# Kernel tuning notes

Measured on AMD Instinct MI355X. Metric: run time of the kernel, lower is better.

## Reference

```python
import jax, jax.numpy as jnp
import numpy as np

B, P, ENC = 64, 196, 2048
ATT, DEC, EMB = 512, 512, 512
V, MAXLEN = 10000, 30


def setup_inputs() -> dict:
    key = jax.random.key(0)
    ks = jax.random.split(key, 20)
    s = 0.02
    inp = {
        "encoder_out": jax.random.normal(ks[0], (B, P, ENC), jnp.float32),
        "captions": jax.random.randint(ks[1], (B, MAXLEN), 0, V).astype(jnp.int64),
        "caption_lengths": jax.random.randint(ks[2], (B,), 1, MAXLEN).astype(jnp.int64),
        # parameters (PyTorch Linear convention: y = x @ W.T + b)
        "emb_table": jax.random.uniform(ks[3], (V, EMB), jnp.float32, -0.1, 0.1),
        "W_enc_att": jax.random.normal(ks[4], (ATT, ENC), jnp.float32) * s,
        "b_enc_att": jnp.zeros((ATT,), jnp.float32),
        "W_dec_att": jax.random.normal(ks[5], (ATT, DEC), jnp.float32) * s,
        "b_dec_att": jnp.zeros((ATT,), jnp.float32),
        "w_full_att": jax.random.normal(ks[6], (1, ATT), jnp.float32) * s,
        "b_full_att": jnp.zeros((1,), jnp.float32),
        "W_ih": jax.random.normal(ks[7], (4 * DEC, EMB + ENC), jnp.float32) * s,
        "b_ih": jnp.zeros((4 * DEC,), jnp.float32),
        "W_hh": jax.random.normal(ks[8], (4 * DEC, DEC), jnp.float32) * s,
        "b_hh": jnp.zeros((4 * DEC,), jnp.float32),
        "W_init_h": jax.random.normal(ks[9], (DEC, ENC), jnp.float32) * s,
        "b_init_h": jnp.zeros((DEC,), jnp.float32),
        "W_init_c": jax.random.normal(ks[10], (DEC, ENC), jnp.float32) * s,
        "b_init_c": jnp.zeros((DEC,), jnp.float32),
        "W_fc": jax.random.uniform(ks[11], (V, DEC), jnp.float32, -0.1, 0.1),
        "b_fc": jnp.zeros((V,), jnp.float32),
    }
    return inp


def reference(encoder_out, captions, caption_lengths, emb_table,
              W_enc_att, b_enc_att, W_dec_att, b_dec_att,
              w_full_att, b_full_att, W_ih, b_ih, W_hh, b_hh,
              W_init_h, b_init_h, W_init_c, b_init_c, W_fc, b_fc):
    # init hidden state from mean-pooled encoder features
    mean_enc = encoder_out.mean(axis=1)                       # [B, ENC]
    h0 = mean_enc @ W_init_h.T + b_init_h                     # [B, DEC]
    c0 = mean_enc @ W_init_c.T + b_init_c                     # [B, DEC]

    # encoder-side attention projection is time-invariant: hoist out of the loop
    att1 = jnp.einsum('bpe,ae->bpa', encoder_out, W_enc_att) + b_enc_att  # [B, P, ATT]

    embeddings = emb_table[captions]                          # [B, T, EMB]
    T = captions.shape[1] - 1
    emb_steps = jnp.swapaxes(embeddings[:, :T, :], 0, 1)      # [T, B, EMB]

    def step(carry, emb_t):
        h, c = carry
        att2 = h @ W_dec_att.T + b_dec_att                    # [B, ATT]
        e = (jax.nn.relu(att1 + att2[:, None, :]) @ w_full_att.T + b_full_att)[..., 0]  # [B, P]
        alpha = jax.nn.softmax(e, axis=1)                     # [B, P]
        context = jnp.einsum('bp,bpe->be', alpha, encoder_out)  # [B, ENC]
        x = jnp.concatenate([emb_t, context], axis=1)         # [B, EMB+ENC]
        gates = x @ W_ih.T + b_ih + h @ W_hh.T + b_hh         # [B, 4*DEC]
        i, f, g, o = jnp.split(gates, 4, axis=1)
        c_new = jax.nn.sigmoid(f) * c + jax.nn.sigmoid(i) * jnp.tanh(g)
        h_new = jax.nn.sigmoid(o) * jnp.tanh(c_new)
        preds = h_new @ W_fc.T + b_fc                         # dropout in eval mode = identity
        return (h_new, c_new), (preds, alpha)

    _, (preds_seq, alpha_seq) = jax.lax.scan(step, (h0, c0), emb_steps)
    predictions = jnp.swapaxes(preds_seq, 0, 1)               # [B, T, V]
    alphas = jnp.swapaxes(alpha_seq, 0, 1)                    # [B, T, P]
    return predictions, alphas
```

## Files before the change

kernel.cpp:

```cpp
#include <hip/hip_runtime.h>
#include <cstddef>

constexpr int B_   = 64;
constexpr int P_   = 196;
constexpr int ENC_ = 2048;
constexpr int ATT_ = 512;
constexpr int DEC_ = 512;
constexpr int EMB_ = 512;
constexpr int V_   = 10000;
constexpr int MAXLEN_ = 30;
constexpr int T_   = 29;
constexpr int G4_  = 2048;
constexpr int KIH_ = 2560;
constexpr int XK2_ = 2560;

constexpr int NBLK = 256;
constexpr int TPB  = 1024;
constexpr int NT   = NBLK * TPB;
constexpr int NW   = NT / 64;
constexpr int FSTR = 16;
constexpr size_t ZS_ = (size_t)B_ * G4_;
constexpr int NPT = 625;

typedef __attribute__((ext_vector_type(8))) short short8;
typedef __attribute__((ext_vector_type(4))) float f32x4;
using us = unsigned short;

__device__ __forceinline__ us f2bf(float x) {
    union { float f; unsigned u; } v; v.f = x;
    unsigned r = v.u + 0x7fff + ((v.u >> 16) & 1);
    return (us)(r >> 16);
}
__device__ __forceinline__ float bf2f(us u) {
    union { unsigned u; float f; } v; v.u = ((unsigned)u) << 16;
    return v.f;
}

__device__ __forceinline__ unsigned ld4cc(const void* p) {
    unsigned r;
    asm volatile("global_load_dword %0, %1, off sc1\n\ts_waitcnt vmcnt(0)"
                 : "=v"(r) : "v"(p) : "memory");
    return r;
}
__device__ __forceinline__ void ld4cc_x8(const float* p0, const float* p1,
                                         const float* p2, const float* p3,
                                         const float* p4, const float* p5,
                                         const float* p6, const float* p7,
                                         float* o) {
    float r0, r1, r2, r3, r4, r5, r6, r7;
    asm volatile("global_load_dword %0, %8, off sc1\n\t"
                 "global_load_dword %1, %9, off sc1\n\t"
                 "global_load_dword %2, %10, off sc1\n\t"
                 "global_load_dword %3, %11, off sc1\n\t"
                 "global_load_dword %4, %12, off sc1\n\t"
                 "global_load_dword %5, %13, off sc1\n\t"
                 "global_load_dword %6, %14, off sc1\n\t"
                 "global_load_dword %7, %15, off sc1\n\t"
                 "s_waitcnt vmcnt(0)"
                 : "=&v"(r0), "=&v"(r1), "=&v"(r2), "=&v"(r3),
                   "=&v"(r4), "=&v"(r5), "=&v"(r6), "=&v"(r7)
                 : "v"(p0), "v"(p1), "v"(p2), "v"(p3),
                   "v"(p4), "v"(p5), "v"(p6), "v"(p7) : "memory");
    o[0]=r0; o[1]=r1; o[2]=r2; o[3]=r3; o[4]=r4; o[5]=r5; o[6]=r6; o[7]=r7;
}
__device__ __forceinline__ void ld16cc_x3(const void* p0, const void* p1, const void* p2,
                                          short8* a, short8* b, short8* c) {
    short8 ra, rb, rc;
    asm volatile("global_load_dwordx4 %0, %3, off sc1\n\t"
                 "global_load_dwordx4 %1, %4, off sc1\n\t"
                 "global_load_dwordx4 %2, %5, off sc1\n\t"
                 "s_waitcnt vmcnt(0)"
                 : "=&v"(ra), "=&v"(rb), "=&v"(rc)
                 : "v"(p0), "v"(p1), "v"(p2) : "memory");
    *a = ra; *b = rb; *c = rc;
}
__device__ __forceinline__ void ld16cc_x4(const void* p0, const void* p1,
                                          const void* p2, const void* p3,
                                          short8* a, short8* b, short8* c, short8* d) {
    short8 ra, rb, rc, rd;
    asm volatile("global_load_dwordx4 %0, %4, off sc1\n\t"
                 "global_load_dwordx4 %1, %5, off sc1\n\t"
                 "global_load_dwordx4 %2, %6, off sc1\n\t"
                 "global_load_dwordx4 %3, %7, off sc1\n\t"
                 "s_waitcnt vmcnt(0)"
                 : "=&v"(ra), "=&v"(rb), "=&v"(rc), "=&v"(rd)
                 : "v"(p0), "v"(p1), "v"(p2), "v"(p3) : "memory");
    *a = ra; *b = rb; *c = rc; *d = rd;
}
__device__ __forceinline__ void ldf8cc(const void* p0, const void* p1, f32x4* a, f32x4* b) {
    f32x4 ra, rb;
    asm volatile("global_load_dwordx4 %0, %2, off sc1\n\t"
                 "global_load_dwordx4 %1, %3, off sc1\n\t"
                 "s_waitcnt vmcnt(0)"
                 : "=&v"(ra), "=&v"(rb) : "v"(p0), "v"(p1) : "memory");
    *a = ra; *b = rb;
}
__device__ __forceinline__ void st4cc(void* p, unsigned v) {
    asm volatile("global_store_dword %0, %1, off sc1" :: "v"(p), "v"(v) : "memory");
}
__device__ __forceinline__ void st2cc(void* p, unsigned v) {
    asm volatile("global_store_short %0, %1, off sc1" :: "v"(p), "v"(v) : "memory");
}
__device__ __forceinline__ float wredsum(float a) {
#pragma unroll
    for (int o = 32; o > 0; o >>= 1) a += __shfl_xor(a, o);
    return a;
}

template<bool REL>
__device__ __forceinline__ void gbar_arrive(unsigned* flags, unsigned tok) {
    asm volatile("s_waitcnt vmcnt(0)" ::: "memory");
    __syncthreads();
    if (threadIdx.x == 0)
        __hip_atomic_store(&flags[blockIdx.x * FSTR], tok,
                           REL ? __ATOMIC_RELEASE : __ATOMIC_RELAXED,
                           __HIP_MEMORY_SCOPE_AGENT);
}
__device__ __forceinline__ void gbar_wait(unsigned* flags, unsigned tok) {
    if (threadIdx.x < NBLK) {
        while (__hip_atomic_load(&flags[threadIdx.x * FSTR], __ATOMIC_RELAXED,
                                 __HIP_MEMORY_SCOPE_AGENT) < tok)
            __builtin_amdgcn_s_sleep(1);
    }
    __syncthreads();
}
template<bool REL>
__device__ __forceinline__ void gbar(unsigned* flags, unsigned tok) {
    gbar_arrive<REL>(flags, tok);
    gbar_wait(flags, tok);
}

__device__ __forceinline__ void cvt8(const float* __restrict__ src, us* __restrict__ dst) {
    const float4* p = (const float4*)src;
    float4 a = p[0], b = p[1];
    union { short8 v; us u[8]; } o;
    o.u[0] = f2bf(a.x); o.u[1] = f2bf(a.y); o.u[2] = f2bf(a.z); o.u[3] = f2bf(a.w);
    o.u[4] = f2bf(b.x); o.u[5] = f2bf(b.y); o.u[6] = f2bf(b.z); o.u[7] = f2bf(b.w);
    *(short8*)dst = o.v;
}

__device__ __forceinline__ float score8(short8 v, const f32x4& lo, const f32x4& hi,
                                        const float4& w0, const float4& w1) {
    float acc = 0.f, x;
    x = bf2f((us)v[0]) + lo[0]; acc += fmaxf(x, 0.f) * w0.x;
    x = bf2f((us)v[1]) + lo[1]; acc += fmaxf(x, 0.f) * w0.y;
    x = bf2f((us)v[2]) + lo[2]; acc += fmaxf(x, 0.f) * w0.z;
    x = bf2f((us)v[3]) + lo[3]; acc += fmaxf(x, 0.f) * w0.w;
    x = bf2f((us)v[4]) + hi[0]; acc += fmaxf(x, 0.f) * w1.x;
    x = bf2f((us)v[5]) + hi[1]; acc += fmaxf(x, 0.f) * w1.y;
    x = bf2f((us)v[6]) + hi[2]; acc += fmaxf(x, 0.f) * w1.z;
    x = bf2f((us)v[7]) + hi[3]; acc += fmaxf(x, 0.f) * w1.w;
    return acc;
}

__device__ __forceinline__ void preds_task(const us* s_h, const us* __restrict__ wfcb,
                                           const float* __restrict__ b_fc,
                                           float* __restrict__ outp,
                                           int nt, int tt, int lane) {
    const int r = lane & 15, g = lane >> 4;
    f32x4 acc[4] = {{0,0,0,0},{0,0,0,0},{0,0,0,0},{0,0,0,0}};
    const us* Brow = wfcb + (size_t)(nt*16 + r)*DEC_ + g*8;
    const us* As   = s_h + r*520 + g*8;
#pragma unroll
    for (int k0 = 0; k0 < DEC_; k0 += 64) {
        short8 b0 = *(const short8*)(Brow + k0);
        short8 b1 = *(const short8*)(Brow + k0 + 32);
#pragma unroll
        for (int mt = 0; mt < 4; ++mt) {
            short8 a0 = *(const short8*)(As + mt*16*520 + k0);
            short8 a1 = *(const short8*)(As + mt*16*520 + k0 + 32);
            acc[mt] = __builtin_amdgcn_mfma_f32_16x16x32_bf16(a0, b0, acc[mt], 0, 0, 0);
            acc[mt] = __builtin_amdgcn_mfma_f32_16x16x32_bf16(a1, b1, acc[mt], 0, 0, 0);
        }
    }
    const int n = nt*16 + r;
    const float bv = b_fc[n];
#pragma unroll
    for (int mt = 0; mt < 4; ++mt)
#pragma unroll
        for (int i = 0; i < 4; ++i) {
            int b = mt*16 + g*4 + i;
            outp[(size_t)b*(T_*V_) + (size_t)tt*V_ + n] = acc[mt][i] + bv;
        }
}

__global__ __launch_bounds__(TPB)
__attribute__((amdgpu_waves_per_eu(4, 4)))
void k_persist(
    const float* __restrict__ enc, const int* __restrict__ captions,
    const float* __restrict__ emb_table,
    const float* __restrict__ W_enc_att, const float* __restrict__ b_enc_att,
    const float* __restrict__ W_dec_att, const float* __restrict__ b_dec_att,
    const float* __restrict__ w_full,
    const float* __restrict__ W_ih, const float* __restrict__ b_ih,
    const float* __restrict__ W_hh, const float* __restrict__ b_hh,
    const float* __restrict__ W_init_h, const float* __restrict__ b_init_h,
    const float* __restrict__ W_init_c, const float* __restrict__ b_init_c,
    const float* __restrict__ W_fc, const float* __restrict__ b_fc,
    us* encb, us* wencb, us* wdecb, us* wfcb, us* wcat2, us* wembW,
    us* winitb, us* xembA, us* att1b, us* hbuf, us* xcatb, us* meanbb,
    float* cst, float* att2G, float* gp, float* gpe, float* bsum,
    unsigned* flags, float* outp, float* outa)
{
    __shared__ us s_stage[64 * 520];
    __shared__ us s_wb[64 * 328];
    __shared__ us s_wd[16 * 520];
    __shared__ float s_e[P_];
    __shared__ float s_al[P_];
    __shared__ float s_red[32];

    const int tid = threadIdx.x, bid = blockIdx.x;
    const int gtid = bid * TPB + tid;
    const int wid  = gtid >> 6;
    const int w    = tid >> 6;
    const int lane = tid & 63;
    unsigned tok = 0;
    float creg = 0.f;
    us* const hb0 = hbuf;
    us* const hb1 = hbuf + (size_t)B_ * DEC_;

    for (int i = gtid; i < B_*P_*ENC_/8; i += NT) cvt8(enc + (size_t)i*8, encb + (size_t)i*8);
    for (int i = gtid; i < ATT_*ENC_/8; i += NT) cvt8(W_enc_att + (size_t)i*8, wencb + (size_t)i*8);
    for (int i = gtid; i < ATT_*DEC_/8; i += NT) cvt8(W_dec_att + (size_t)i*8, wdecb + (size_t)i*8);
    for (int i = gtid; i < V_*DEC_/8;   i += NT) cvt8(W_fc + (size_t)i*8, wfcb + (size_t)i*8);
    for (int i = gtid; i < G4_*XK2_/8;  i += NT) {
        int n = (i*8) / XK2_, k = (i*8) % XK2_;
        const float* src = (k < ENC_) ? (W_ih + (size_t)n*KIH_ + EMB_ + k)
                                      : (W_hh + (size_t)n*DEC_ + (k - ENC_));
        cvt8(src, wcat2 + (size_t)i*8);
    }
    for (int i = gtid; i < G4_*EMB_/8;  i += NT)
        cvt8(W_ih + ((size_t)((i*8) / EMB_))*KIH_ + ((i*8) % EMB_), wembW + (size_t)i*8);
    for (int i = gtid; i < 1024*ENC_/8; i += NT) {
        int n = (i*8) >> 11, k = (i*8) & (ENC_ - 1);
        const float* src = (n < 512) ? (W_init_h + (size_t)n*ENC_ + k)
                                     : (W_init_c + (size_t)(n-512)*ENC_ + k);
        cvt8(src, winitb + (size_t)i*8);
    }
    for (int i = gtid; i < T_*B_*EMB_/8; i += NT) {
        int r = i >> 6, c8 = i & 63;
        int t = r >> 6, b = r & 63;
        int cap = captions[b*MAXLEN_ + t];
        cvt8(emb_table + (size_t)cap*EMB_ + c8*8, xembA + (size_t)r*EMB_ + c8*8);
    }
    if (gtid < G4_) bsum[gtid] = b_ih[gtid] + b_hh[gtid];
    if (gtid < B_*ENC_) {
        int b = gtid >> 11, e = gtid & (ENC_ - 1);
        const float* base = enc + (size_t)b*P_*ENC_ + e;
        float s = 0.f;
        for (int p = 0; p < P_; ++p) s += base[(size_t)p*ENC_];
        meanbb[gtid] = f2bf(s * (1.f / P_));
    }
    gbar<true>(flags, ++tok);

    for (int task = wid; task < 256 + 1856; task += NW) {
        const int r = lane & 15, g = lane >> 4;
        if (task < 256) {
            const int mt = task & 3, nt = task >> 2;
            const int m0 = mt*16, n0 = nt*16;
            const us* Ar = meanbb + (size_t)(m0 + r)*ENC_ + g*8;
            const us* Br = winitb + (size_t)(n0 + r)*ENC_ + g*8;
            f32x4 acc0 = {0,0,0,0}, acc1 = {0,0,0,0};
#pragma unroll 4
            for (int k0 = 0; k0 < ENC_; k0 += 64) {
                acc0 = __builtin_amdgcn_mfma_f32_16x16x32_bf16(
                    *(const short8*)(Ar + k0), *(const short8*)(Br + k0), acc0, 0, 0, 0);
                acc1 = __builtin_amdgcn_mfma_f32_16x16x32_bf16(
                    *(const short8*)(Ar + k0 + 32), *(const short8*)(Br + k0 + 32), acc1, 0, 0, 0);
            }
            const int n = n0 + r;
            if (n < 512) {
                float bv = b_init_h[n];
#pragma unroll
                for (int i = 0; i < 4; ++i) {
                    int b = m0 + g*4 + i;
                    unsigned hv = f2bf(acc0[i] + acc1[i] + bv);
                    st2cc(hb1 + b*DEC_ + n, hv);
                    st2cc(xcatb + (size_t)b*XK2_ + ENC_ + n, hv);
                }
            } else {
                int d = n - 512;
                float bv = b_init_c[d];
#pragma unroll
                for (int i = 0; i < 4; ++i)
                    st4cc(cst + (m0 + g*4 + i)*DEC_ + d,
                          __float_as_uint(acc0[i] + acc1[i] + bv));
            }
        } else {
            const int q = task - 256;
            const int m0 = (q >> 6) * 64, n0 = (q & 63) * 32;
            f32x4 acc[4][2] = {};
            const us* Ab = xembA + (size_t)(m0 + r)*EMB_ + g*8;
            const us* Bb = wembW + (size_t)(n0 + r)*EMB_ + g*8;
#pragma unroll 2
            for (int k0 = 0; k0 < EMB_; k0 += 32) {
                short8 af[4], bfr[2];
#pragma unroll
                for (int mi = 0; mi < 4; ++mi)
                    af[mi] = *(const short8*)(Ab + (size_t)mi*16*EMB_ + k0);
#pragma unroll
                for (int nj = 0; nj < 2; ++nj)
                    bfr[nj] = *(const short8*)(Bb + (size_t)nj*16*EMB_ + k0);
#pragma unroll
                for (int mi = 0; mi < 4; ++mi)
#pragma unroll
                    for (int nj = 0; nj < 2; ++nj)
                        acc[mi][nj] = __builtin_amdgcn_mfma_f32_16x16x32_bf16(
                            af[mi], bfr[nj], acc[mi][nj], 0, 0, 0);
            }
#pragma unroll
            for (int mi = 0; mi < 4; ++mi)
#pragma unroll
                for (int nj = 0; nj < 2; ++nj) {
                    int n = n0 + nj*16 + r;
                    float bv = bsum[n];
#pragma unroll
                    for (int i = 0; i < 4; ++i) {
                        int m = m0 + mi*16 + g*4 + i;
                        gpe[(size_t)m*G4_ + n] = acc[mi][nj][i] + bv;
                    }
                }
        }
    }
    gbar<true>(flags, ++tok);

    for (int task = wid; task < 3264; task += NW) {
        const int r = lane & 15, g = lane >> 4;
        if (task < 3136) {
            int mt = task >> 4, nt2 = task & 15;
            int m0 = mt*64, n0 = nt2*32;
            f32x4 acc[4][2] = {};
            const us* Ab = encb + (size_t)(m0 + r)*ENC_ + g*8;
            const us* Bb = wencb + (size_t)(n0 + r)*ENC_ + g*8;
#pragma unroll 2
            for (int k0 = 0; k0 < ENC_; k0 += 32) {
                short8 af[4], bfr[2];
#pragma unroll
                for (int mi = 0; mi < 4; ++mi)
                    af[mi] = *(const short8*)(Ab + (size_t)mi*16*ENC_ + k0);
#pragma unroll
                for (int nj = 0; nj < 2; ++nj)
                    bfr[nj] = *(const short8*)(Bb + (size_t)nj*16*ENC_ + k0);
#pragma unroll
                for (int mi = 0; mi < 4; ++mi)
#pragma unroll
                    for (int nj = 0; nj < 2; ++nj)
                        acc[mi][nj] = __builtin_amdgcn_mfma_f32_16x16x32_bf16(
                            af[mi], bfr[nj], acc[mi][nj], 0, 0, 0);
            }
#pragma unroll
            for (int mi = 0; mi < 4; ++mi)
#pragma unroll
                for (int nj = 0; nj < 2; ++nj) {
                    int n = n0 + nj*16 + r;
                    float bv = b_enc_att[n];
#pragma unroll
                    for (int i = 0; i < 4; ++i) {
                        int m = m0 + mi*16 + g*4 + i;
                        att1b[(size_t)m*ATT_ + n] = f2bf(acc[mi][nj][i] + bv);
                    }
                }
        } else {
            int q = task - 3136;
            int nt = q >> 2, mt = q & 3;
            const us* Ar = hb1 + (size_t)(mt*16 + r)*DEC_ + g*8;
            const us* Br = wdecb + (size_t)(nt*16 + r)*DEC_ + g*8;
            f32x4 acc0 = {0,0,0,0}, acc1 = {0,0,0,0};
#pragma unroll 4
            for (int k0 = 0; k0 < DEC_; k0 += 64) {
                short8 a0, a1, dum;
                ld16cc_x3(Ar + k0, Ar + k0 + 32, Ar + k0, &a0, &a1, &dum);
                acc0 = __builtin_amdgcn_mfma_f32_16x16x32_bf16(
                    a0, *(const short8*)(Br + k0), acc0, 0, 0, 0);
                acc1 = __builtin_amdgcn_mfma_f32_16x16x32_bf16(
                    a1, *(const short8*)(Br + k0 + 32), acc1, 0, 0, 0);
            }
            int n = nt*16 + r;
            float bv = b_dec_att[n];
#pragma unroll
            for (int i = 0; i < 4; ++i)
                st4cc(att2G + (size_t)(mt*16 + g*4 + i)*ATT_ + n,
                      __float_as_uint(acc0[i] + acc1[i] + bv));
        }
    }
    gbar<true>(flags, ++tok);

    {
        const int z = bid >> 5, nb = bid & 31;
        for (int c = tid; c < 2560; c += TPB) {
            int row = c / 40, col8 = c % 40;
            *(short8*)(s_wb + row*328 + col8*8) =
                *(const short8*)(wcat2 + (size_t)(nb*64 + row)*XK2_ + (size_t)z*320 + col8*8);
        }
        if (bid < 32)
            for (int c = tid; c < 1024; c += TPB) {
                int row = c >> 6, col8 = c & 63;
                *(short8*)(s_wd + row*520 + col8*8) =
                    *(const short8*)(wdecb + (size_t)(bid*16 + row)*DEC_ + col8*8);
            }
        if (tid < 128) creg = __uint_as_float(ld4cc(cst + bid*128 + tid));
        __syncthreads();
    }

    for (int t = 0; t < T_; ++t) {
        {
            const int b = bid & 63, cc = bid >> 6;
            f32x4 a2lo, a2hi;
            const float* ap = att2G + (size_t)b*ATT_ + lane*8;
            ldf8cc(ap, ap + 4, &a2lo, &a2hi);
            const float4 w0 = *(const float4*)(w_full + lane*8);
            const float4 w1 = *(const float4*)(w_full + lane*8 + 4);
            const us* a1base = att1b + (size_t)b*P_*ATT_ + lane*8;
            for (int p = w; p < P_; p += 32) {
                const int p2 = p + 16;
                short8 v0 = *(const short8*)(a1base + (size_t)p*ATT_);
                short8 v1 = (p2 < P_) ? *(const short8*)(a1base + (size_t)p2*ATT_) : v0;
                float acc0 = score8(v0, a2lo, a2hi, w0, w1);
                float acc1 = score8(v1, a2lo, a2hi, w0, w1);
                acc0 = wredsum(acc0);
                acc1 = wredsum(acc1);
                if (lane == 0) {
                    s_e[p] = acc0;
                    if (p2 < P_) s_e[p2] = acc1;
                }
            }
            __syncthreads();
            float v = (tid < P_) ? s_e[tid] : -3.4e38f;
            float mx = v;
#pragma unroll
            for (int o = 32; o > 0; o >>= 1) mx = fmaxf(mx, __shfl_xor(mx, o));
            if (lane == 0) s_red[w] = mx;
            __syncthreads();
            mx = s_red[0];
#pragma unroll
            for (int j = 1; j < 16; ++j) mx = fmaxf(mx, s_red[j]);
            float ev = (tid < P_) ? expf(v - mx) : 0.f;
            float sm = wredsum(ev);
            if (lane == 0) s_red[16 + w] = sm;
            __syncthreads();
            float tot = 0.f;
#pragma unroll
            for (int j = 0; j < 16; ++j) tot += s_red[16 + j];
            if (tid < P_) {
                float al = ev / tot;
                s_al[tid] = al;
                if (cc == 0) outa[((size_t)b*T_ + t)*P_ + tid] = al;
            }
            __syncthreads();
            float a[8] = {};
            const us* ep = encb + (size_t)b*P_*ENC_ + cc*512 + lane*8;
            for (int p = w; p < P_; p += 16) {
                short8 vv = *(const short8*)(ep + (size_t)p*ENC_);
                float al = s_al[p];
#pragma unroll
                for (int j = 0; j < 8; ++j) a[j] += al * bf2f((us)vv[j]);
            }
            float* s_accf = (float*)s_stage;
            {
                f32x4 lo = {a[0],a[1],a[2],a[3]}, hi = {a[4],a[5],a[6],a[7]};
                *(f32x4*)(s_accf + w*512 + lane*8)     = lo;
                *(f32x4*)(s_accf + w*512 + lane*8 + 4) = hi;
            }
            __syncthreads();
            if (tid < 256) {
                int c2 = tid*2;
                float s0 = 0.f, s1 = 0.f;
#pragma unroll
                for (int q = 0; q < 16; ++q) {
                    s0 += s_accf[q*512 + c2];
                    s1 += s_accf[q*512 + c2 + 1];
                }
                unsigned pk = (unsigned)f2bf(s0) | ((unsigned)f2bf(s1) << 16);
                st4cc(xcatb + (size_t)b*XK2_ + cc*512 + c2, pk);
            }
            __syncthreads();
        }
        gbar<false>(flags, ++tok);

        {
            const int z = bid >> 5;
            {
                short8 v0, v1, v2;
                int c0 = tid, c1 = tid + 1024, c2i = tid + 2048;
                const us* p0 = xcatb + (size_t)(c0/40)*XK2_ + z*320 + (c0%40)*8;
                const us* p1 = xcatb + (size_t)(c1/40)*XK2_ + z*320 + (c1%40)*8;
                bool has2 = c2i < 2560;
                const us* p2 = has2 ? xcatb + (size_t)(c2i/40)*XK2_ + z*320 + (c2i%40)*8 : p0;
                ld16cc_x3(p0, p1, p2, &v0, &v1, &v2);
                *(short8*)(s_stage + (c0/40)*328 + (c0%40)*8) = v0;
                *(short8*)(s_stage + (c1/40)*328 + (c1%40)*8) = v1;
                if (has2) *(short8*)(s_stage + (c2i/40)*328 + (c2i%40)*8) = v2;
            }
            __syncthreads();
            const int nt = (bid & 31)*4 + (w >> 2), mt = w & 3;
            const int r = lane & 15, g = lane >> 4;
            const us* sxr = s_stage + (mt*16 + r)*328 + g*8;
            const us* Br  = s_wb + ((w >> 2)*16 + r)*328 + g*8;
            f32x4 acc0 = {0,0,0,0}, acc1 = {0,0,0,0};
#pragma unroll
            for (int k0 = 0; k0 < 320; k0 += 64) {
                acc0 = __builtin_amdgcn_mfma_f32_16x16x32_bf16(
                    *(const short8*)(sxr + k0), *(const short8*)(Br + k0), acc0, 0, 0, 0);
                acc1 = __builtin_amdgcn_mfma_f32_16x16x32_bf16(
                    *(const short8*)(sxr + k0 + 32), *(const short8*)(Br + k0 + 32), acc1, 0, 0, 0);
            }
            const int n = nt*16 + r;
#pragma unroll
            for (int i = 0; i < 4; ++i) {
                int m = mt*16 + g*4 + i;
                st4cc(gp + ZS_*z + (size_t)m*G4_ + n, __float_as_uint(acc0[i] + acc1[i]));
            }
            __syncthreads();
        }
        gbar<false>(flags, ++tok);

        {
            float* sg = (float*)s_stage;
            if (tid < 512) {
                const int cell = tid & 127, gate = tid >> 7;
                const int idx = bid*128 + cell;
                const int b = idx >> 9, d = idx & 511;
                const float* gz = gp + (size_t)b*G4_ + gate*512 + d;
                float vz[8];
                ld4cc_x8(gz, gz + ZS_, gz + 2*ZS_, gz + 3*ZS_,
                         gz + 4*ZS_, gz + 5*ZS_, gz + 6*ZS_, gz + 7*ZS_, vz);
                sg[tid] = ((vz[0]+vz[1]) + (vz[2]+vz[3])) + ((vz[4]+vz[5]) + (vz[6]+vz[7]));
            }
            __syncthreads();
            if (tid < 128) {
                const int idx = bid*128 + tid;
                const int b = idx >> 9, d = idx & 511;
                const float* ge = gpe + ((size_t)(t*B_ + b))*G4_ + d;
                float gi = sg[tid]       + ge[0];
                float gf = sg[128 + tid] + ge[512];
                float gg = sg[256 + tid] + ge[1024];
                float go = sg[384 + tid] + ge[1536];
                float si = 1.f / (1.f + expf(-gi));
                float sf = 1.f / (1.f + expf(-gf));
                float so = 1.f / (1.f + expf(-go));
                float cn = sf * creg + si * tanhf(gg);
                creg = cn;
                float hn = so * tanhf(cn);
                unsigned hv = f2bf(hn);
                us* hnew = (t & 1) ? hb1 : hb0;
                st2cc(hnew + idx, hv);
                st2cc(xcatb + (size_t)b*XK2_ + ENC_ + d, hv);
            }
        }
        gbar<false>(flags, ++tok);

        if (t != T_ - 1) {
            ++tok;
            if (bid < 32) {
                {
                    const us* hbn = (t & 1) ? hb1 : hb0;
                    short8 v0, v1, v2, v3;
                    int c0 = tid, c1 = tid + 1024, c2i = tid + 2048, c3 = tid + 3072;
                    ld16cc_x4(hbn + (c0>>6)*DEC_ + (c0&63)*8, hbn + (c1>>6)*DEC_ + (c1&63)*8,
                              hbn + (c2i>>6)*DEC_ + (c2i&63)*8, hbn + (c3>>6)*DEC_ + (c3&63)*8,
                              &v0, &v1, &v2, &v3);
                    *(short8*)(s_stage + (c0>>6)*520 + (c0&63)*8) = v0;
                    *(short8*)(s_stage + (c1>>6)*520 + (c1&63)*8) = v1;
                    *(short8*)(s_stage + (c2i>>6)*520 + (c2i&63)*8) = v2;
                    *(short8*)(s_stage + (c3>>6)*520 + (c3&63)*8) = v3;
                }
                __syncthreads();
                if (w < 4) {
                    const int r = lane & 15, g = lane >> 4;
                    const us* As = s_stage + (w*16 + r)*520 + g*8;
                    const us* Bs = s_wd + r*520 + g*8;
                    f32x4 acc0 = {0,0,0,0}, acc1 = {0,0,0,0};
#pragma unroll
                    for (int k0 = 0; k0 < DEC_; k0 += 64) {
                        acc0 = __builtin_amdgcn_mfma_f32_16x16x32_bf16(
                            *(const short8*)(As + k0), *(const short8*)(Bs + k0), acc0, 0, 0, 0);
                        acc1 = __builtin_amdgcn_mfma_f32_16x16x32_bf16(
                            *(const short8*)(As + k0 + 32), *(const short8*)(Bs + k0 + 32), acc1, 0, 0, 0);
                    }
                    const int n = bid*16 + r;
                    float bv = b_dec_att[n];
#pragma unroll
                    for (int i = 0; i < 4; ++i)
                        st4cc(att2G + (size_t)(w*16 + g*4 + i)*ATT_ + n,
                              __float_as_uint(acc0[i] + acc1[i] + bv));
                }
                gbar_arrive<false>(flags, tok);
                gbar_wait(flags, tok);
            } else {
                gbar_arrive<false>(flags, tok);
                if (t > 0) {
                    const us* hbo = (t & 1) ? hb0 : hb1;
                    short8 v0, v1, v2, v3;
                    int c0 = tid, c1 = tid + 1024, c2i = tid + 2048, c3 = tid + 3072;
                    ld16cc_x4(hbo + (c0>>6)*DEC_ + (c0&63)*8, hbo + (c1>>6)*DEC_ + (c1&63)*8,
                              hbo + (c2i>>6)*DEC_ + (c2i&63)*8, hbo + (c3>>6)*DEC_ + (c3&63)*8,
                              &v0, &v1, &v2, &v3);
                    *(short8*)(s_stage + (c0>>6)*520 + (c0&63)*8) = v0;
                    *(short8*)(s_stage + (c1>>6)*520 + (c1&63)*8) = v1;
                    *(short8*)(s_stage + (c2i>>6)*520 + (c2i&63)*8) = v2;
                    *(short8*)(s_stage + (c3>>6)*520 + (c3&63)*8) = v3;
                    __syncthreads();
                    const int tq = (bid - 32)*3 + w;
                    if (w < 3 && tq < NPT)
                        preds_task(s_stage, wfcb, b_fc, outp, tq, t - 1, lane);
                }
                gbar_wait(flags, tok);
            }
        } else {
            if (bid >= 32) {
                const us* hbo = (t & 1) ? hb0 : hb1;
                short8 v0, v1, v2, v3;
                int c0 = tid, c1 = tid + 1024, c2i = tid + 2048, c3 = tid + 3072;
                ld16cc_x4(hbo + (c0>>6)*DEC_ + (c0&63)*8, hbo + (c1>>6)*DEC_ + (c1&63)*8,
                          hbo + (c2i>>6)*DEC_ + (c2i&63)*8, hbo + (c3>>6)*DEC_ + (c3&63)*8,
                          &v0, &v1, &v2, &v3);
                *(short8*)(s_stage + (c0>>6)*520 + (c0&63)*8) = v0;
                *(short8*)(s_stage + (c1>>6)*520 + (c1&63)*8) = v1;
                *(short8*)(s_stage + (c2i>>6)*520 + (c2i&63)*8) = v2;
                *(short8*)(s_stage + (c3>>6)*520 + (c3&63)*8) = v3;
                __syncthreads();
                const int tq = (bid - 32)*3 + w;
                if (w < 3 && tq < NPT)
                    preds_task(s_stage, wfcb, b_fc, outp, tq, t - 1, lane);
            }
        }
    }

    if (bid < 40) {
        __syncthreads();
        const us* hbn = ((T_ - 1) & 1) ? hb1 : hb0;
        {
            short8 v0, v1, v2, v3;
            int c0 = tid, c1 = tid + 1024, c2i = tid + 2048, c3 = tid + 3072;
            ld16cc_x4(hbn + (c0>>6)*DEC_ + (c0&63)*8, hbn + (c1>>6)*DEC_ + (c1&63)*8,
                      hbn + (c2i>>6)*DEC_ + (c2i&63)*8, hbn + (c3>>6)*DEC_ + (c3&63)*8,
                      &v0, &v1, &v2, &v3);
            *(short8*)(s_stage + (c0>>6)*520 + (c0&63)*8) = v0;
            *(short8*)(s_stage + (c1>>6)*520 + (c1&63)*8) = v1;
            *(short8*)(s_stage + (c2i>>6)*520 + (c2i&63)*8) = v2;
            *(short8*)(s_stage + (c3>>6)*520 + (c3&63)*8) = v3;
        }
        __syncthreads();
        const int tq = bid*16 + w;
        if (tq < NPT)
            preds_task(s_stage, wfcb, b_fc, outp, tq, T_ - 1, lane);
    }
}

extern "C" void kernel_launch(void* const* d_in, const int* in_sizes, int n_in,
                              void* d_out, int out_size, void* d_ws, size_t ws_size,
                              hipStream_t stream) {
    const float* enc       = (const float*)d_in[0];
    const int*   captions  = (const int*)d_in[1];
    const float* emb_table = (const float*)d_in[3];
    const float* W_enc_att = (const float*)d_in[4];
    const float* b_enc_att = (const float*)d_in[5];
    const float* W_dec_att = (const float*)d_in[6];
    const float* b_dec_att = (const float*)d_in[7];
    const float* w_full    = (const float*)d_in[8];
    const float* W_ih      = (const float*)d_in[10];
    const float* b_ih      = (const float*)d_in[11];
    const float* W_hh      = (const float*)d_in[12];
    const float* b_hh      = (const float*)d_in[13];
    const float* W_init_h  = (const float*)d_in[14];
    const float* b_init_h  = (const float*)d_in[15];
    const float* W_init_c  = (const float*)d_in[16];
    const float* b_init_c  = (const float*)d_in[17];
    const float* W_fc      = (const float*)d_in[18];
    const float* b_fc      = (const float*)d_in[19];

    char* ws = (char*)d_ws;
    size_t off = 0;
    auto alloc = [&](size_t bytes) {
        void* p = ws + off;
        off = (off + bytes + 255) & ~(size_t)255;
        return p;
    };
    us* encb   = (us*)alloc((size_t)B_ * P_ * ENC_ * 2);
    us* wencb  = (us*)alloc((size_t)ATT_ * ENC_ * 2);
    us* wdecb  = (us*)alloc((size_t)ATT_ * DEC_ * 2);
    us* wfcb   = (us*)alloc((size_t)V_ * DEC_ * 2);
    us* wcat2  = (us*)alloc((size_t)G4_ * XK2_ * 2);
    us* wembW  = (us*)alloc((size_t)G4_ * EMB_ * 2);
    us* winitb = (us*)alloc((size_t)1024 * ENC_ * 2);
    us* xembA  = (us*)alloc((size_t)T_ * B_ * EMB_ * 2);
    us* att1b  = (us*)alloc((size_t)B_ * P_ * ATT_ * 2);
    us* hbuf   = (us*)alloc((size_t)2 * B_ * DEC_ * 2);
    us* xcatb  = (us*)alloc((size_t)B_ * XK2_ * 2);
    us* meanbb = (us*)alloc((size_t)B_ * ENC_ * 2);
    float* cst   = (float*)alloc((size_t)B_ * DEC_ * 4);
    float* att2G = (float*)alloc((size_t)B_ * ATT_ * 4);
    float* gp    = (float*)alloc((size_t)B_ * G4_ * 8 * 4);
    float* gpe   = (float*)alloc((size_t)T_ * B_ * G4_ * 4);
    float* bsum  = (float*)alloc((size_t)G4_ * 4);
    unsigned* flags = (unsigned*)alloc((size_t)(NBLK + 1) * FSTR * 4);

    float* outp = (float*)d_out;
    float* outa = outp + (size_t)B_ * T_ * V_;

    hipMemsetAsync(flags, 0, (NBLK + 1) * FSTR * sizeof(unsigned), stream);
    k_persist<<<NBLK, TPB, 0, stream>>>(
        enc, captions, emb_table, W_enc_att, b_enc_att, W_dec_att, b_dec_att,
        w_full, W_ih, b_ih, W_hh, b_hh, W_init_h, b_init_h, W_init_c, b_init_c,
        W_fc, b_fc,
        encb, wencb, wdecb, wfcb, wcat2, wembW, winitb, xembA, att1b, hbuf, xcatb,
        meanbb, cst, att2G, gp, gpe, bsum, flags, outp, outa);
}
```

Baseline: 1.200 ms.

## Replace end-of-step grid barrier with per-block att2 readiness flags

New measurement: 1.198 ms (median of 2 runs). Within noise of the previous version (-0.1%).

```diff
diff --git a/kernel.cpp b/kernel.cpp
--- a/kernel.cpp
+++ b/kernel.cpp
@@ -185,7 +185,6 @@
 }
 
 __global__ __launch_bounds__(TPB)
-__attribute__((amdgpu_waves_per_eu(4, 4)))
 void k_persist(
     const float* __restrict__ enc, const int* __restrict__ captions,
     const float* __restrict__ emb_table,
@@ -218,6 +217,7 @@
     float creg = 0.f;
     us* const hb0 = hbuf;
     us* const hb1 = hbuf + (size_t)B_ * DEC_;
+    unsigned* const aflags = flags + (NBLK + 16) * FSTR;
 
     for (int i = gtid; i < B_*P_*ENC_/8; i += NT) cvt8(enc + (size_t)i*8, encb + (size_t)i*8);
     for (int i = gtid; i < ATT_*ENC_/8; i += NT) cvt8(W_enc_att + (size_t)i*8, wencb + (size_t)i*8);
@@ -401,22 +401,30 @@
         if (tid < 128) creg = __uint_as_float(ld4cc(cst + bid*128 + tid));
         __syncthreads();
     }
+    const float4 w0v = *(const float4*)(w_full + lane*8);
+    const float4 w1v = *(const float4*)(w_full + lane*8 + 4);
 
     for (int t = 0; t < T_; ++t) {
         {
+            if (t > 0) {
+                if (tid < 32) {
+                    while (__hip_atomic_load(&aflags[tid * FSTR], __ATOMIC_RELAXED,
+                                             __HIP_MEMORY_SCOPE_AGENT) < (unsigned)t)
+                        __builtin_amdgcn_s_sleep(1);
+                }
+                __syncthreads();
+            }
             const int b = bid & 63, cc = bid >> 6;
             f32x4 a2lo, a2hi;
             const float* ap = att2G + (size_t)b*ATT_ + lane*8;
             ldf8cc(ap, ap + 4, &a2lo, &a2hi);
-            const float4 w0 = *(const float4*)(w_full + lane*8);
-            const float4 w1 = *(const float4*)(w_full + lane*8 + 4);
             const us* a1base = att1b + (size_t)b*P_*ATT_ + lane*8;
             for (int p = w; p < P_; p += 32) {
                 const int p2 = p + 16;
                 short8 v0 = *(const short8*)(a1base + (size_t)p*ATT_);
                 short8 v1 = (p2 < P_) ? *(const short8*)(a1base + (size_t)p2*ATT_) : v0;
-                float acc0 = score8(v0, a2lo, a2hi, w0, w1);
-                float acc1 = score8(v1, a2lo, a2hi, w0, w1);
+                float acc0 = score8(v0, a2lo, a2hi, w0v, w1v);
+                float acc1 = score8(v1, a2lo, a2hi, w0v, w1v);
                 acc0 = wredsum(acc0);
                 acc1 = wredsum(acc1);
                 if (lane == 0) {
@@ -549,21 +557,18 @@
         }
         gbar<false>(flags, ++tok);
 
-        if (t != T_ - 1) {
-            ++tok;
-            if (bid < 32) {
-                {
-                    const us* hbn = (t & 1) ? hb1 : hb0;
-                    short8 v0, v1, v2, v3;
-                    int c0 = tid, c1 = tid + 1024, c2i = tid + 2048, c3 = tid + 3072;
-                    ld16cc_x4(hbn + (c0>>6)*DEC_ + (c0&63)*8, hbn + (c1>>6)*DEC_ + (c1&63)*8,
-                              hbn + (c2i>>6)*DEC_ + (c2i&63)*8, hbn + (c3>>6)*DEC_ + (c3&63)*8,
-                              &v0, &v1, &v2, &v3);
-                    *(short8*)(s_stage + (c0>>6)*520 + (c0&63)*8) = v0;
-                    *(short8*)(s_stage + (c1>>6)*520 + (c1&63)*8) = v1;
-                    *(short8*)(s_stage + (c2i>>6)*520 + (c2i&63)*8) = v2;
-                    *(short8*)(s_stage + (c3>>6)*520 + (c3&63)*8) = v3;
-                }
+        if (bid < 32) {
+            if (t != T_ - 1) {
+                const us* hbn = (t & 1) ? hb1 : hb0;
+                short8 v0, v1, v2, v3;
+                int c0 = tid, c1 = tid + 1024, c2i = tid + 2048, c3 = tid + 3072;
+                ld16cc_x4(hbn + (c0>>6)*DEC_ + (c0&63)*8, hbn + (c1>>6)*DEC_ + (c1&63)*8,
+                          hbn + (c2i>>6)*DEC_ + (c2i&63)*8, hbn + (c3>>6)*DEC_ + (c3&63)*8,
+                          &v0, &v1, &v2, &v3);
+                *(short8*)(s_stage + (c0>>6)*520 + (c0&63)*8) = v0;
+                *(short8*)(s_stage + (c1>>6)*520 + (c1&63)*8) = v1;
+                *(short8*)(s_stage + (c2i>>6)*520 + (c2i&63)*8) = v2;
+                *(short8*)(s_stage + (c3>>6)*520 + (c3&63)*8) = v3;
                 __syncthreads();
                 if (w < 4) {
                     const int r = lane & 15, g = lane >> 4;
@@ -584,45 +589,28 @@
                         st4cc(att2G + (size_t)(w*16 + g*4 + i)*ATT_ + n,
                               __float_as_uint(acc0[i] + acc1[i] + bv));
                 }
-                gbar_arrive<false>(flags, tok);
-                gbar_wait(flags, tok);
-            } else {
-                gbar_arrive<false>(flags, tok);
-                if (t > 0) {
-                    const us* hbo = (t & 1) ? hb0 : hb1;
-                    short8 v0, v1, v2, v3;
-                    int c0 = tid, c1 = tid + 1024, c2i = tid + 2048, c3 = tid + 3072;
-                    ld16cc_x4(hbo + (c0>>6)*DEC_ + (c0&63)*8, hbo + (c1>>6)*DEC_ + (c1&63)*8,
-                              hbo + (c2i>>6)*DEC_ + (c2i&63)*8, hbo + (c3>>6)*DEC_ + (c3&63)*8,
-                              &v0, &v1, &v2, &v3);
-                    *(short8*)(s_stage + (c0>>6)*520 + (c0&63)*8) = v0;
-                    *(short8*)(s_stage + (c1>>6)*520 + (c1&63)*8) = v1;
-                    *(short8*)(s_stage + (c2i>>6)*520 + (c2i&63)*8) = v2;
-                    *(short8*)(s_stage + (c3>>6)*520 + (c3&63)*8) = v3;
-                    __syncthreads();
-                    const int tq = (bid - 32)*3 + w;
-                    if (w < 3 && tq < NPT)
-                        preds_task(s_stage, wfcb, b_fc, outp, tq, t - 1, lane);
-                }
-                gbar_wait(flags, tok);
-            }
-        } else {
-            if (bid >= 32) {
-                const us* hbo = (t & 1) ? hb0 : hb1;
-                short8 v0, v1, v2, v3;
-                int c0 = tid, c1 = tid + 1024, c2i = tid + 2048, c3 = tid + 3072;
-                ld16cc_x4(hbo + (c0>>6)*DEC_ + (c0&63)*8, hbo + (c1>>6)*DEC_ + (c1&63)*8,
-                          hbo + (c2i>>6)*DEC_ + (c2i&63)*8, hbo + (c3>>6)*DEC_ + (c3&63)*8,
-                          &v0, &v1, &v2, &v3);
-                *(short8*)(s_stage + (c0>>6)*520 + (c0&63)*8) = v0;
-                *(short8*)(s_stage + (c1>>6)*520 + (c1&63)*8) = v1;
-                *(short8*)(s_stage + (c2i>>6)*520 + (c2i&63)*8) = v2;
-                *(short8*)(s_stage + (c3>>6)*520 + (c3&63)*8) = v3;
+                asm volatile("s_waitcnt vmcnt(0)" ::: "memory");
                 __syncthreads();
-                const int tq = (bid - 32)*3 + w;
-                if (w < 3 && tq < NPT)
-                    preds_task(s_stage, wfcb, b_fc, outp, tq, t - 1, lane);
-            }
+                if (tid == 0)
+                    __hip_atomic_store(&aflags[bid * FSTR], (unsigned)(t + 1),
+                                       __ATOMIC_RELAXED, __HIP_MEMORY_SCOPE_AGENT);
+            }
+        } else if (t > 0) {
+            const us* hbo = (t & 1) ? hb0 : hb1;
+            short8 v0, v1, v2, v3;
+            int c0 = tid, c1 = tid + 1024, c2i = tid + 2048, c3 = tid + 3072;
+            ld16cc_x4(hbo + (c0>>6)*DEC_ + (c0&63)*8, hbo + (c1>>6)*DEC_ + (c1&63)*8,
+                      hbo + (c2i>>6)*DEC_ + (c2i&63)*8, hbo + (c3>>6)*DEC_ + (c3&63)*8,
+                      &v0, &v1, &v2, &v3);
+            *(short8*)(s_stage + (c0>>6)*520 + (c0&63)*8) = v0;
+            *(short8*)(s_stage + (c1>>6)*520 + (c1&63)*8) = v1;
+            *(short8*)(s_stage + (c2i>>6)*520 + (c2i&63)*8) = v2;
+            *(short8*)(s_stage + (c3>>6)*520 + (c3&63)*8) = v3;
+            __syncthreads();
+            const int tq = (bid - 32)*3 + w;
+            if (w < 3 && tq < NPT)
+                preds_task(s_stage, wfcb, b_fc, outp, tq, t - 1, lane);
+            __syncthreads();
         }
     }
 
@@ -693,12 +681,12 @@
     float* gp    = (float*)alloc((size_t)B_ * G4_ * 8 * 4);
     float* gpe   = (float*)alloc((size_t)T_ * B_ * G4_ * 4);
     float* bsum  = (float*)alloc((size_t)G4_ * 4);
-    unsigned* flags = (unsigned*)alloc((size_t)(NBLK + 1) * FSTR * 4);
+    unsigned* flags = (unsigned*)alloc((size_t)(NBLK + 64) * FSTR * 4);
 
     float* outp = (float*)d_out;
     float* outa = outp + (size_t)B_ * T_ * V_;
 
-    hipMemsetAsync(flags, 0, (NBLK + 1) * FSTR * sizeof(unsigned), stream);
+    hipMemsetAsync(flags, 0, (NBLK + 64) * FSTR * sizeof(unsigned), stream);
     k_persist<<<NBLK, TPB, 0, stream>>>(
         enc, captions, emb_table, W_enc_att, b_enc_att, W_dec_att, b_dec_att,
         w_full, W_ih, b_ih, W_hh, b_hh, W_init_h, b_init_h, W_init_c, b_init_c,
```
